# Performance work log

Measured on AMD Instinct MI355X. Metric: run time of the kernel, lower is better.

## Reference

```python
import jax, jax.numpy as jnp
import numpy as np


def setup_inputs() -> dict:
    key = jax.random.key(0)
    ip = jax.random.normal(key, (8, 256, 128, 128), dtype=jnp.float32)
    return {"ip": ip}


def reference(ip):
    b, C, H, W = ip.shape
    two_c = 2 * C
    # precomputed complex shift grid: exp(-1j*2*pi*(C-0.5)*v/(2C)), v = 0..2C-1
    v = jnp.arange(two_c, dtype=jnp.float32)
    angle = -2.0 * jnp.pi * (C - 0.5) * v / two_c
    shift = (jnp.cos(angle) + 1j * jnp.sin(angle)).astype(jnp.complex64)  # [2C]

    viDct = ip * two_c                                   # [b, C, H, W]
    flip_neg = -viDct[:, 1:][:, ::-1]                    # [b, C-1, H, W]
    zeros = jnp.zeros((b, 1, H, W), dtype=ip.dtype)
    rev = jnp.concatenate([viDct, zeros, flip_neg], axis=1)  # [b, 2C, H, W]
    rev = rev.astype(jnp.complex64) * shift[None, :, None, None]
    vxx = jnp.fft.ifft(rev, axis=1)                      # norm='backward' (default)
    out = vxx[:, :C][:, ::-1].real                       # first C, flipped, real part
    return out.astype(ip.dtype)
```

## Files before the change

### kernel.cpp

```cpp
#include <hip/hip_runtime.h>
#include <hip/hip_bf16.h>
#include <math.h>

#define NB   8
#define NC   256
#define NHW  (128 * 128)

#define BM 128
#define BN 128
#define BK 32
#define LSTR 80

typedef __attribute__((ext_vector_type(4))) float f32x4;
typedef __attribute__((ext_vector_type(8))) short bf16x8;

__device__ __forceinline__ unsigned short f2bf(float f) {
    unsigned u = __builtin_bit_cast(unsigned, f);
    u += 0x7fffu + ((u >> 16) & 1u);
    return (unsigned short)(u >> 16);
}

__global__ void coef_kernel(unsigned short* __restrict__ coef) {
    int idx = blockIdx.x * 256 + threadIdx.x;
    int c = idx >> 8;
    int k = idx & 255;
    int t = (k * (2 * c + 1)) & 1023;
    float v = (k == 0) ? 1.0f : 2.0f * cosf((float)t * (float)(M_PI / 512.0));
    coef[idx] = f2bf(v);
}

__global__ __launch_bounds__(256, 2)
void dct_gemm(const float* __restrict__ X, const unsigned short* __restrict__ Mcoef,
              float* __restrict__ Out) {
    __shared__ unsigned char lds[2 * BM * LSTR];
    unsigned char* Alds = lds;
    unsigned char* Xlds = lds + BM * LSTR;

    const int tid  = threadIdx.x;
    const int lane = tid & 63;
    const int wave = tid >> 6;
    const int wm   = wave >> 1;
    const int wn   = wave & 1;
    const int m16  = lane & 15;
    const int quad = lane >> 4;

    const int p0 = blockIdx.x * BN;
    const int c0 = blockIdx.y * BM;
    const int bbase = blockIdx.z * (NC * NHW);

    const float* Xb = X + bbase;
    float* Ob = Out + bbase;

    const int sr = tid & 127;
    const int sh = tid >> 7;

    f32x4 acc[4][4];
#pragma unroll
    for (int i = 0; i < 4; i++)
#pragma unroll
        for (int j = 0; j < 4; j++) acc[i][j] = (f32x4){0.f, 0.f, 0.f, 0.f};

    for (int k0 = 0; k0 < NC; k0 += BK) {
        __syncthreads();

        {
            const unsigned short* src = Mcoef + (c0 + sr) * NC + k0 + sh * 16;
            int4 a0 = *(const int4*)(src);
            int4 a1 = *(const int4*)(src + 8);
            unsigned char* dst = Alds + sr * LSTR + sh * 32;
            *(int4*)(dst)      = a0;
            *(int4*)(dst + 16) = a1;
        }

        {
            const float* src = Xb + (k0 + sh * 16) * NHW + p0 + sr;
            float v[16];
#pragma unroll
            for (int j = 0; j < 16; j++) v[j] = src[j * NHW];
            unsigned pk[8];
#pragma unroll
            for (int j = 0; j < 8; j++) {
                unsigned lo = __builtin_bit_cast(unsigned, v[2 * j]);
                lo += 0x7fffu + ((lo >> 16) & 1u);
                unsigned hi = __builtin_bit_cast(unsigned, v[2 * j + 1]);
                hi += 0x7fffu + ((hi >> 16) & 1u);
                pk[j] = (lo >> 16) | (hi & 0xffff0000u);
            }
            unsigned char* dst = Xlds + sr * LSTR + sh * 32;
            *(int4*)(dst)      = (int4){(int)pk[0], (int)pk[1], (int)pk[2], (int)pk[3]};
            *(int4*)(dst + 16) = (int4){(int)pk[4], (int)pk[5], (int)pk[6], (int)pk[7]};
        }

        __syncthreads();

        bf16x8 afrag[4], bfrag[4];
#pragma unroll
        for (int mt = 0; mt < 4; mt++) {
            int row = wm * 64 + mt * 16 + m16;
            afrag[mt] = *(const bf16x8*)(Alds + row * LSTR + quad * 16);
        }
#pragma unroll
        for (int nt = 0; nt < 4; nt++) {
            int row = wn * 64 + nt * 16 + m16;
            bfrag[nt] = *(const bf16x8*)(Xlds + row * LSTR + quad * 16);
        }
#pragma unroll
        for (int mt = 0; mt < 4; mt++)
#pragma unroll
            for (int nt = 0; nt < 4; nt++)
                acc[mt][nt] = __builtin_amdgcn_mfma_f32_16x16x32_bf16(
                    afrag[mt], bfrag[nt], acc[mt][nt], 0, 0, 0);
    }

#pragma unroll
    for (int mt = 0; mt < 4; mt++) {
#pragma unroll
        for (int nt = 0; nt < 4; nt++) {
            int cc = c0 + wm * 64 + mt * 16 + quad * 4;
            int pp = p0 + wn * 64 + nt * 16 + m16;
            float* o = Ob + cc * NHW + pp;
#pragma unroll
            for (int r = 0; r < 4; r++)
                o[r * NHW] = acc[mt][nt][r];
        }
    }
}

extern "C" void kernel_launch(void* const* d_in, const int* in_sizes, int n_in,
                              void* d_out, int out_size, void* d_ws, size_t ws_size,
                              hipStream_t stream) {
    const float* ip = (const float*)d_in[0];
    float* out = (float*)d_out;
    unsigned short* coef = (unsigned short*)d_ws;

    coef_kernel<<<dim3(256), dim3(256), 0, stream>>>(coef);

    dim3 grid(NHW / BN, NC / BM, NB);
    dct_gemm<<<grid, dim3(256), 0, stream>>>(ip, coef, out);
}
```

Baseline: 247.5 us.

## Double-buffer LDS with async coefficient loads, swizzled layout, and smaller N tile

Restructures the DCT-as-GEMM kernel to double-buffer LDS. The next K-slice of X is prefetched into registers and the coefficient tile is fetched directly into LDS with global_load_lds while MFMAs run on the current buffer, leaving one barrier per iteration. Padding is replaced with an XOR swizzle to avoid LDS bank conflicts. BN drops to 64 with occupancy hint 4, and output stores become nontemporal. The smaller tile doubles the number of coefficient-tile loads and adds swizzle address arithmetic.

After: 259.6 us. 4.9% more time.

```diff
diff --git a/kernel.cpp b/kernel.cpp
--- a/kernel.cpp
+++ b/kernel.cpp
@@ -1,5 +1,4 @@
 #include <hip/hip_runtime.h>
-#include <hip/hip_bf16.h>
 #include <math.h>
 
 #define NB   8
@@ -7,9 +6,9 @@
 #define NHW  (128 * 128)
 
 #define BM 128
-#define BN 128
+#define BN 64
 #define BK 32
-#define LSTR 80
+#define NITER (NC / BK)
 
 typedef __attribute__((ext_vector_type(4))) float f32x4;
 typedef __attribute__((ext_vector_type(8))) short bf16x8;
@@ -18,6 +17,14 @@
     unsigned u = __builtin_bit_cast(unsigned, f);
     u += 0x7fffu + ((u >> 16) & 1u);
     return (unsigned short)(u >> 16);
+}
+
+__device__ __forceinline__ unsigned pack2bf(float a, float b) {
+    unsigned lo = __builtin_bit_cast(unsigned, a);
+    lo += 0x7fffu + ((lo >> 16) & 1u);
+    unsigned hi = __builtin_bit_cast(unsigned, b);
+    hi += 0x7fffu + ((hi >> 16) & 1u);
+    return (lo >> 16) | (hi & 0xffff0000u);
 }
 
 __global__ void coef_kernel(unsigned short* __restrict__ coef) {
@@ -29,99 +36,122 @@
     coef[idx] = f2bf(v);
 }
 
-__global__ __launch_bounds__(256, 2)
+__device__ __forceinline__ void gload_lds16(const void* g, void* l) {
+    __builtin_amdgcn_global_load_lds(
+        (const __attribute__((address_space(1))) unsigned int*)g,
+        (__attribute__((address_space(3))) unsigned int*)l,
+        16, 0, 0);
+}
+
+
+__global__ __launch_bounds__(256, 4)
 void dct_gemm(const float* __restrict__ X, const unsigned short* __restrict__ Mcoef,
               float* __restrict__ Out) {
-    __shared__ unsigned char lds[2 * BM * LSTR];
-    unsigned char* Alds = lds;
-    unsigned char* Xlds = lds + BM * LSTR;
+    __shared__ __align__(16) unsigned char lds[24576];
 
     const int tid  = threadIdx.x;
     const int lane = tid & 63;
     const int wave = tid >> 6;
+    const int m16  = lane & 15;
+    const int quad = lane >> 4;
     const int wm   = wave >> 1;
     const int wn   = wave & 1;
-    const int m16  = lane & 15;
-    const int quad = lane >> 4;
 
     const int p0 = blockIdx.x * BN;
     const int c0 = blockIdx.y * BM;
-    const int bbase = blockIdx.z * (NC * NHW);
+    const size_t bbase = (size_t)blockIdx.z * (NC * NHW);
+    const float* Xg = X + bbase;
+    float* Og = Out + bbase;
 
-    const float* Xb = X + bbase;
-    float* Ob = Out + bbase;
+    const int bA0 = wave * 2048 + lane * 16;
+    const int bA1 = bA0 + 1024;
+    const int rA0 = bA0 >> 6, rA1 = bA1 >> 6;
+    const int qA0 = ((bA0 >> 4) & 3) ^ ((rA0 >> 1) & 3);
+    const int qA1 = ((bA1 >> 4) & 3) ^ ((rA1 >> 1) & 3);
+    const unsigned short* aSrc0 = Mcoef + (c0 + rA0) * NC + qA0 * 8;
+    const unsigned short* aSrc1 = Mcoef + (c0 + rA1) * NC + qA1 * 8;
 
-    const int sr = tid & 127;
-    const int sh = tid >> 7;
+    const int sp = lane;
+    const float* xSrc = Xg + (size_t)(wave * 8) * NHW + p0 + sp;
+    const int xWoff = sp * 64 + ((wave ^ ((sp >> 1) & 3)) << 4);
 
-    f32x4 acc[4][4];
+    int offA[4], offB[2];
+#pragma unroll
+    for (int mt = 0; mt < 4; mt++) {
+        int r = wm * 64 + mt * 16 + m16;
+        offA[mt] = r * 64 + ((quad ^ ((r >> 1) & 3)) << 4);
+    }
+#pragma unroll
+    for (int nt = 0; nt < 2; nt++) {
+        int r = wn * 32 + nt * 16 + m16;
+        offB[nt] = r * 64 + ((quad ^ ((r >> 1) & 3)) << 4);
+    }
+
+    f32x4 acc[4][2];
 #pragma unroll
     for (int i = 0; i < 4; i++)
 #pragma unroll
-        for (int j = 0; j < 4; j++) acc[i][j] = (f32x4){0.f, 0.f, 0.f, 0.f};
+        for (int j = 0; j < 2; j++) acc[i][j] = (f32x4){0.f, 0.f, 0.f, 0.f};
 
-    for (int k0 = 0; k0 < NC; k0 += BK) {
-        __syncthreads();
+    {
+        float xv[8];
+#pragma unroll
+        for (int j = 0; j < 8; j++) xv[j] = xSrc[(size_t)j * NHW];
+        gload_lds16(aSrc0, lds + 0 + bA0);
+        gload_lds16(aSrc1, lds + 0 + bA1);
+        int4 w = { (int)pack2bf(xv[0], xv[1]), (int)pack2bf(xv[2], xv[3]),
+                   (int)pack2bf(xv[4], xv[5]), (int)pack2bf(xv[6], xv[7]) };
+        *(int4*)(lds + 16384 + xWoff) = w;
+    }
+    __syncthreads();
 
-        {
-            const unsigned short* src = Mcoef + (c0 + sr) * NC + k0 + sh * 16;
-            int4 a0 = *(const int4*)(src);
-            int4 a1 = *(const int4*)(src + 8);
-            unsigned char* dst = Alds + sr * LSTR + sh * 32;
-            *(int4*)(dst)      = a0;
-            *(int4*)(dst + 16) = a1;
+#pragma unroll
+    for (int t = 0; t < NITER; t++) {
+        const int cb = t & 1;
+        const unsigned char* Ac = lds + (cb ? 8192 : 0);
+        const unsigned char* Xc = lds + 16384 + (cb ? 4096 : 0);
+        unsigned char* As = lds + (cb ? 0 : 8192);
+        unsigned char* Xs = lds + 16384 + (cb ? 0 : 4096);
+
+        float xv[8];
+        if (t + 1 < NITER) {
+            const int k0 = (t + 1) * BK;
+#pragma unroll
+            for (int j = 0; j < 8; j++) xv[j] = xSrc[(size_t)(k0 + j) * NHW];
+            gload_lds16(aSrc0 + k0, As + bA0);
+            gload_lds16(aSrc1 + k0, As + bA1);
         }
 
-        {
-            const float* src = Xb + (k0 + sh * 16) * NHW + p0 + sr;
-            float v[16];
+        bf16x8 af[4], bfr[2];
 #pragma unroll
-            for (int j = 0; j < 16; j++) v[j] = src[j * NHW];
-            unsigned pk[8];
+        for (int mt = 0; mt < 4; mt++) af[mt] = *(const bf16x8*)(Ac + offA[mt]);
 #pragma unroll
-            for (int j = 0; j < 8; j++) {
-                unsigned lo = __builtin_bit_cast(unsigned, v[2 * j]);
-                lo += 0x7fffu + ((lo >> 16) & 1u);
-                unsigned hi = __builtin_bit_cast(unsigned, v[2 * j + 1]);
-                hi += 0x7fffu + ((hi >> 16) & 1u);
-                pk[j] = (lo >> 16) | (hi & 0xffff0000u);
-            }
-            unsigned char* dst = Xlds + sr * LSTR + sh * 32;
-            *(int4*)(dst)      = (int4){(int)pk[0], (int)pk[1], (int)pk[2], (int)pk[3]};
-            *(int4*)(dst + 16) = (int4){(int)pk[4], (int)pk[5], (int)pk[6], (int)pk[7]};
-        }
-
-        __syncthreads();
-
-        bf16x8 afrag[4], bfrag[4];
-#pragma unroll
-        for (int mt = 0; mt < 4; mt++) {
-            int row = wm * 64 + mt * 16 + m16;
-            afrag[mt] = *(const bf16x8*)(Alds + row * LSTR + quad * 16);
-        }
-#pragma unroll
-        for (int nt = 0; nt < 4; nt++) {
-            int row = wn * 64 + nt * 16 + m16;
-            bfrag[nt] = *(const bf16x8*)(Xlds + row * LSTR + quad * 16);
-        }
+        for (int nt = 0; nt < 2; nt++) bfr[nt] = *(const bf16x8*)(Xc + offB[nt]);
 #pragma unroll
         for (int mt = 0; mt < 4; mt++)
 #pragma unroll
-            for (int nt = 0; nt < 4; nt++)
+            for (int nt = 0; nt < 2; nt++)
                 acc[mt][nt] = __builtin_amdgcn_mfma_f32_16x16x32_bf16(
-                    afrag[mt], bfrag[nt], acc[mt][nt], 0, 0, 0);
+                    af[mt], bfr[nt], acc[mt][nt], 0, 0, 0);
+
+        if (t + 1 < NITER) {
+            int4 w = { (int)pack2bf(xv[0], xv[1]), (int)pack2bf(xv[2], xv[3]),
+                       (int)pack2bf(xv[4], xv[5]), (int)pack2bf(xv[6], xv[7]) };
+            *(int4*)(Xs + xWoff) = w;
+            __syncthreads();
+        }
     }
 
 #pragma unroll
     for (int mt = 0; mt < 4; mt++) {
+        const int cc = c0 + wm * 64 + mt * 16 + quad * 4;
 #pragma unroll
-        for (int nt = 0; nt < 4; nt++) {
-            int cc = c0 + wm * 64 + mt * 16 + quad * 4;
-            int pp = p0 + wn * 64 + nt * 16 + m16;
-            float* o = Ob + cc * NHW + pp;
+        for (int nt = 0; nt < 2; nt++) {
+            const int pp = p0 + wn * 32 + nt * 16 + m16;
+            float* o = Og + (size_t)cc * NHW + pp;
 #pragma unroll
             for (int r = 0; r < 4; r++)
-                o[r * NHW] = acc[mt][nt][r];
+                __builtin_nontemporal_store(acc[mt][nt][r], o + (size_t)r * NHW);
         }
     }
 }
```
